# Performance work log

Measured on AMD Instinct MI355X. Metric: run time of the kernel, lower is better.

## Reference

```python
import jax, jax.numpy as jnp
import numpy as np

N_NODES = 100000
N_EDGES = 1600000
NUM_GRAPHS = 4096
HID = 128
F_IN = 11
F_OUT = 19


def setup_inputs() -> dict:
    key = jax.random.key(0)
    ks = jax.random.split(key, 8)
    x = jax.random.normal(ks[0], (N_NODES, F_IN), dtype=jnp.float32)
    edge_src = jax.random.randint(ks[1], (N_EDGES,), 0, N_NODES)
    edge_dst = jax.random.randint(ks[2], (N_EDGES,), 0, N_NODES)
    batch = jnp.sort(jax.random.randint(ks[3], (N_NODES,), 0, NUM_GRAPHS))
    W1 = jax.random.normal(ks[4], (F_IN, HID), dtype=jnp.float32) / np.sqrt(F_IN)
    b1 = jnp.zeros((HID,), dtype=jnp.float32)
    W2 = jax.random.normal(ks[5], (HID, HID), dtype=jnp.float32) / np.sqrt(HID)
    b2 = jnp.zeros((HID,), dtype=jnp.float32)
    Wlin = jax.random.normal(ks[6], (HID, F_OUT), dtype=jnp.float32) / np.sqrt(HID)
    blin = jnp.zeros((F_OUT,), dtype=jnp.float32)
    return {"x": x, "edge_src": edge_src, "edge_dst": edge_dst, "batch": batch,
            "W1": W1, "b1": b1, "W2": W2, "b2": b2, "Wlin": Wlin, "blin": blin}


def _gcn_conv(x, W, b, src, dst, norm, n_nodes):
    # x: [N, Fin] -> h: [N, Fout]; gather-normalize-scatter over edges (self-loops included in src/dst/norm)
    h = x @ W
    msgs = h[src] * norm[:, None]              # [E+N, Fout]
    out = jax.ops.segment_sum(msgs, dst, num_segments=n_nodes)
    return out + b


def reference(x, edge_src, edge_dst, batch, W1, b1, W2, b2, Wlin, blin):
    n = x.shape[0]
    # add self-loops (GCNConv default)
    loops = jnp.arange(n)
    src = jnp.concatenate([edge_src, loops])
    dst = jnp.concatenate([edge_dst, loops])
    # symmetric normalization deg^-1/2[src] * deg^-1/2[dst], deg computed on dst with self-loops
    deg = jax.ops.segment_sum(jnp.ones_like(dst, dtype=x.dtype), dst, num_segments=n)
    dinv = jnp.where(deg > 0, jax.lax.rsqrt(deg), 0.0)
    norm = dinv[src] * dinv[dst]
    h = _gcn_conv(x, W1, b1, src, dst, norm, n)
    h = jax.nn.relu(h)
    h = _gcn_conv(h, W2, b2, src, dst, norm, n)
    # global mean pool over batch assignment
    sums = jax.ops.segment_sum(h, batch, num_segments=NUM_GRAPHS)
    cnts = jax.ops.segment_sum(jnp.ones((n,), dtype=h.dtype), batch, num_segments=NUM_GRAPHS)
    pooled = sums / jnp.maximum(cnts, 1.0)[:, None]   # [NUM_GRAPHS, HID]
    return pooled @ Wlin + blin                       # [NUM_GRAPHS, F_OUT]
```

## Files before the change

kernel.cpp:

```cpp
#include <hip/hip_runtime.h>
#include <hip/hip_fp16.h>

#define N_NODES 100000
#define N_EDGES 1600000
#define NUM_G   4096
#define HID     128
#define F_IN    11
#define F_PAD   16
#define F_OUT   19

#define NB      256
#define KPB     391
#define BCAP    8192
#define GCAP    1024
#define P01_EPB 2048
#define NREG    8
#define REGW    12500
#define GPB     4
#define NAGG    782
#define CH_G    8

__device__ inline void acc_row_f16(float* acc, uint4 u, float w) {
    const __half2* hp = (const __half2*)&u;
#pragma unroll
    for (int i = 0; i < 4; ++i) {
        acc[2 * i]     += __half2float(__low2half(hp[i]))  * w;
        acc[2 * i + 1] += __half2float(__high2half(hp[i])) * w;
    }
}
__device__ inline void add_row_f16(float* acc, uint4 u) {
    const __half2* hp = (const __half2*)&u;
#pragma unroll
    for (int i = 0; i < 4; ++i) {
        acc[2 * i]     += __half2float(__low2half(hp[i]));
        acc[2 * i + 1] += __half2float(__high2half(hp[i]));
    }
}

__global__ void p1_place(const int* __restrict__ src, const int* __restrict__ dst,
                         int* __restrict__ bcur, unsigned int* __restrict__ ebuf) {
    __shared__ int h[NB];
    __shared__ int base[NB];
    h[threadIdx.x] = 0;
    __syncthreads();
    unsigned int pk[8]; int bn[8];
    int b0 = blockIdx.x * P01_EPB;
    int e8 = b0 + threadIdx.x * 8;
    if (e8 + 8 <= N_EDGES) {
        int4 s0 = *(const int4*)(src + e8);
        int4 s1 = *(const int4*)(src + e8 + 4);
        int4 d0 = *(const int4*)(dst + e8);
        int4 d1 = *(const int4*)(dst + e8 + 4);
        int ss[8] = { s0.x, s0.y, s0.z, s0.w, s1.x, s1.y, s1.z, s1.w };
        int dd[8] = { d0.x, d0.y, d0.z, d0.w, d1.x, d1.y, d1.z, d1.w };
#pragma unroll
        for (int k = 0; k < 8; ++k) {
            bn[k] = dd[k] / KPB;
            pk[k] = ((unsigned)ss[k] << 9) | (unsigned)(dd[k] - bn[k] * KPB);
        }
    } else {
#pragma unroll
        for (int k = 0; k < 8; ++k) {
            int e = e8 + k;
            if (e < N_EDGES) {
                int d = dst[e];
                bn[k] = d / KPB;
                pk[k] = ((unsigned)src[e] << 9) | (unsigned)(d - bn[k] * KPB);
            } else bn[k] = -1;
        }
    }
#pragma unroll
    for (int k = 0; k < 8; ++k)
        if (bn[k] >= 0) atomicAdd(&h[bn[k]], 1);
    __syncthreads();
    {
        int c = h[threadIdx.x];
        base[threadIdx.x] = c ? atomicAdd(&bcur[threadIdx.x], c) : 0;
    }
    __syncthreads();
    h[threadIdx.x] = 0;
    __syncthreads();
#pragma unroll
    for (int k = 0; k < 8; ++k) {
        if (bn[k] >= 0) {
            int r = atomicAdd(&h[bn[k]], 1);
            ebuf[(size_t)bn[k] * BCAP + base[bn[k]] + r] = pk[k];
        }
    }
}

__global__ void p2_build(const unsigned int* __restrict__ ebuf, const int* __restrict__ bcur,
                         const float* __restrict__ x,
                         int* __restrict__ row_ptr, int* __restrict__ deg,
                         int* __restrict__ col, float* __restrict__ wd,
                         float* __restrict__ dinv, __half* __restrict__ xp) {
    __shared__ int hist[512];
    __shared__ float ldinv[512];
    __shared__ int wsum[8];
    __shared__ int woff[8];
    int b  = blockIdx.x;
    int t  = threadIdx.x;
    int dbase = b * KPB;
    int nd = N_NODES - dbase; if (nd > KPB) nd = KPB;
    hist[t] = 0;
    __syncthreads();
    int e0 = b * BCAP;
    int e1 = e0 + bcur[b];
    for (int e = e0 + t; e < e1; e += 512)
        atomicAdd(&hist[ebuf[e] & 511u], 1);
    __syncthreads();
    int v = hist[t];
    int lane = t & 63, wv = t >> 6;
    int sv = v;
#pragma unroll
    for (int off = 1; off < 64; off <<= 1) {
        int n = __shfl_up(sv, off, 64);
        if (lane >= off) sv += n;
    }
    if (lane == 63) wsum[wv] = sv;
    __syncthreads();
    if (t == 0) {
        int run = 0;
#pragma unroll
        for (int w = 0; w < 8; ++w) { woff[w] = run; run += wsum[w]; }
    }
    __syncthreads();
    int excl = sv - v + woff[wv];
    float di = rsqrtf(1.0f + (float)v);
    ldinv[t] = di;
    if (t < nd) {
        row_ptr[dbase + t] = e0 + excl;
        deg[dbase + t]     = v;
        dinv[dbase + t]    = di;
    }
    __syncthreads();
    hist[t] = e0 + excl;
    __syncthreads();
    for (int e = e0 + t; e < e1; e += 512) {
        unsigned int w = ebuf[e];
        int dl = (int)(w & 511u);
        int pos = atomicAdd(&hist[dl], 1);
        col[pos] = (int)(w >> 9);
        wd[pos]  = ldinv[dl];
    }
    for (int idx = t; idx < nd * F_PAD; idx += 512) {
        int vl = idx >> 4, f = idx & 15;
        int gv = dbase + vl;
        xp[(size_t)gv * F_PAD + f] =
            __float2half_rn((f < F_IN) ? ldinv[vl] * x[(size_t)gv * F_IN + f] : 0.f);
    }
}

__global__ void agg_es8(const __half* __restrict__ xp, const int* __restrict__ row_ptr,
                        const int* __restrict__ deg, const int* __restrict__ col,
                        const float* __restrict__ dinv,
                        const float* __restrict__ W1, const float* __restrict__ b1,
                        __half* __restrict__ Bh,
                        const int* __restrict__ batch, const float* __restrict__ wd,
                        uint2* __restrict__ ewp, int* __restrict__ gro,
                        int* __restrict__ gb) {
    __shared__ float xs[128][F_PAD];
    __shared__ float W1s[F_IN * HID];
    __shared__ float b1s[HID];
    __shared__ float ds[128];
    __shared__ int cnt[NREG];
    __shared__ int cur[NREG];
    __shared__ int range[2];
    int tid = threadIdx.x;

    if (blockIdx.x < NAGG) {
        for (int i = tid; i < F_IN * HID; i += 256) W1s[i] = W1[i];
        if (tid < HID) b1s[tid] = b1[tid];
        const uint4* xp4 = (const uint4*)xp;
        int v0   = blockIdx.x * 128;
        int v    = v0 + (tid >> 1);
        int lane = tid & 1;
        if (v < N_NODES) {
            if (lane == 0) ds[tid >> 1] = dinv[v];
            float a[8];
#pragma unroll
            for (int k = 0; k < 8; ++k) a[k] = 0.f;
            add_row_f16(a, xp4[(size_t)v * 2 + lane]);
            int j = row_ptr[v], end = j + deg[v];
            for (; j + 3 < end; j += 4) {
                int s0 = col[j], s1 = col[j + 1], s2 = col[j + 2], s3 = col[j + 3];
                uint4 u0 = xp4[(size_t)s0 * 2 + lane];
                uint4 u1 = xp4[(size_t)s1 * 2 + lane];
                uint4 u2 = xp4[(size_t)s2 * 2 + lane];
                uint4 u3 = xp4[(size_t)s3 * 2 + lane];
                add_row_f16(a, u0); add_row_f16(a, u1);
                add_row_f16(a, u2); add_row_f16(a, u3);
            }
            for (; j < end; ++j)
                add_row_f16(a, xp4[(size_t)col[j] * 2 + lane]);
#pragma unroll
            for (int k = 0; k < 8; ++k) xs[tid >> 1][lane * 8 + k] = a[k];
        }
        __syncthreads();
        int jf   = tid & 127;
        int half = tid >> 7;
        int nmax = N_NODES - v0; if (nmax > 128) nmax = 128;
        for (int n = half; n < nmax; n += 2) {
            float a = 0.f;
#pragma unroll
            for (int k = 0; k < F_IN; ++k) a += xs[n][k] * W1s[k * HID + jf];
            float dv = ds[n];
            float h = fmaxf(dv * a + b1s[jf], 0.f);
            Bh[(size_t)(v0 + n) * HID + jf] = __float2half_rn(dv * h);
        }
    } else {
        int g = blockIdx.x - NAGG;
        if (tid < NREG) cnt[tid] = 0;
        if (tid < 2) {
            int tgt = g + tid;
            int lo = 0, hi = N_NODES;
            while (lo < hi) { int m = (lo + hi) >> 1; if (batch[m] < tgt) lo = m + 1; else hi = m; }
            range[tid] = lo;
        }
        __syncthreads();
        int r0 = range[0], r1 = range[1];
        if (tid == 0) {
            gb[g] = r0;
            if (g == NUM_G - 1) gb[NUM_G] = N_NODES;
        }
        int bb0 = 0, bb1 = -1;
        if (r1 > r0) { bb0 = r0 / KPB; bb1 = (r1 - 1) / KPB; }
        for (int bb = bb0; bb <= bb1; ++bb) {
            int vlo = r0 > bb * KPB ? r0 : bb * KPB;
            int vhi = r1 < bb * KPB + KPB ? r1 : bb * KPB + KPB;
            int ee0 = row_ptr[vlo];
            int ee1 = row_ptr[vhi - 1] + deg[vhi - 1];
            for (int e = ee0 + tid; e < ee1; e += 256)
                atomicAdd(&cnt[(unsigned)col[e] / REGW], 1);
        }
        for (int v = r0 + tid; v < r1; v += 256)
            atomicAdd(&cnt[(unsigned)v / REGW], 1);
        __syncthreads();
        if (tid == 0) {
            int run = g * GCAP;
#pragma unroll
            for (int p = 0; p < NREG; ++p) {
                gro[g * 9 + p] = run;
                cur[p] = run;
                run += cnt[p];
            }
            gro[g * 9 + 8] = run;
        }
        __syncthreads();
        for (int bb = bb0; bb <= bb1; ++bb) {
            int vlo = r0 > bb * KPB ? r0 : bb * KPB;
            int vhi = r1 < bb * KPB + KPB ? r1 : bb * KPB + KPB;
            int ee0 = row_ptr[vlo];
            int ee1 = row_ptr[vhi - 1] + deg[vhi - 1];
            for (int e = ee0 + tid; e < ee1; e += 256) {
                int s = col[e];
                int pos = atomicAdd(&cur[(unsigned)s / REGW], 1);
                ewp[pos] = make_uint2((unsigned)s, __float_as_uint(wd[e]));
            }
        }
        for (int v = r0 + tid; v < r1; v += 256) {
            int pos = atomicAdd(&cur[(unsigned)v / REGW], 1);
            ewp[pos] = make_uint2((unsigned)v, __float_as_uint(dinv[v]));
        }
    }
}

__global__ void pool_gather(const __half* __restrict__ Bh,
                            const int* __restrict__ gro,
                            const uint2* __restrict__ ewp,
                            float* __restrict__ part) {
    __shared__ float red[32][HID + 4];
    int b    = blockIdx.x;
    int gset = b >> 3;
    int p    = b & 7;
    int tid  = threadIdx.x;
    int grp  = tid >> 3;
    int lane = tid & 7;
    int g    = gset * GPB + (grp >> 3);
    int q    = grp & 7;
    const uint4* B4 = (const uint4*)Bh;
    float acc[16];
#pragma unroll
    for (int k = 0; k < 16; ++k) acc[k] = 0.f;

    int e0 = gro[g * 9 + p], e1 = gro[g * 9 + p + 1];
    int e = e0 + q;
    for (; e + 24 < e1; e += 32) {
        uint2 q0 = ewp[e], q1 = ewp[e + 8], q2 = ewp[e + 16], q3 = ewp[e + 24];
        uint4 u00 = B4[(size_t)q0.x * 16 + lane];
        uint4 u01 = B4[(size_t)q0.x * 16 + 8 + lane];
        uint4 u10 = B4[(size_t)q1.x * 16 + lane];
        uint4 u11 = B4[(size_t)q1.x * 16 + 8 + lane];
        uint4 u20 = B4[(size_t)q2.x * 16 + lane];
        uint4 u21 = B4[(size_t)q2.x * 16 + 8 + lane];
        uint4 u30 = B4[(size_t)q3.x * 16 + lane];
        uint4 u31 = B4[(size_t)q3.x * 16 + 8 + lane];
        float w0 = __uint_as_float(q0.y), w1 = __uint_as_float(q1.y);
        float w2 = __uint_as_float(q2.y), w3 = __uint_as_float(q3.y);
        acc_row_f16(acc,     u00, w0);
        acc_row_f16(acc + 8, u01, w0);
        acc_row_f16(acc,     u10, w1);
        acc_row_f16(acc + 8, u11, w1);
        acc_row_f16(acc,     u20, w2);
        acc_row_f16(acc + 8, u21, w2);
        acc_row_f16(acc,     u30, w3);
        acc_row_f16(acc + 8, u31, w3);
    }
    for (; e < e1; e += 8) {
        uint2 q0 = ewp[e];
        uint4 u00 = B4[(size_t)q0.x * 16 + lane];
        uint4 u01 = B4[(size_t)q0.x * 16 + 8 + lane];
        float w0 = __uint_as_float(q0.y);
        acc_row_f16(acc,     u00, w0);
        acc_row_f16(acc + 8, u01, w0);
    }
#pragma unroll
    for (int k = 0; k < 8; ++k) red[grp][lane * 8 + k]      = acc[k];
#pragma unroll
    for (int k = 0; k < 8; ++k) red[grp][64 + lane * 8 + k] = acc[8 + k];
    __syncthreads();
    for (int i = tid; i < GPB * HID; i += 256) {
        int gg = i >> 7, f = i & 127;
        int rb = gg * 8;
        float s = 0.f;
#pragma unroll
        for (int r = 0; r < 8; ++r) s += red[rb + r][f];
        part[(size_t)((gset * GPB + gg) * NREG + p) * HID + f] = s;
    }
}

__global__ void combine_head(const float* __restrict__ part, const int* __restrict__ gb,
                             const float* __restrict__ W2, const float* __restrict__ b2,
                             const float* __restrict__ Wlin, const float* __restrict__ blin,
                             float* __restrict__ out) {
    __shared__ float r[CH_G][HID];
    __shared__ float tt[CH_G][HID + 4];
    __shared__ float bsc[CH_G];
    int g0  = blockIdx.x * CH_G;
    int tid = threadIdx.x;
    int f   = tid & 127;
    int gh  = tid >> 7;
    int q0  = gh * 4;
#pragma unroll
    for (int c = 0; c < 4; ++c) {
        int gg = q0 + c;
        int g  = g0 + gg;
        float s = 0.f;
#pragma unroll
        for (int p = 0; p < NREG; ++p) s += part[(size_t)(g * NREG + p) * HID + f];
        int cnt = gb[g + 1] - gb[g];
        float inv = (cnt > 0) ? 1.0f / (float)cnt : 0.f;
        r[gg][f] = s * inv;
        if (f == 0) bsc[gg] = (cnt > 0) ? 1.0f : 0.f;
    }
    __syncthreads();
    float bf = b2[f];
    float t0 = bf * bsc[q0];
    float t1 = bf * bsc[q0 + 1];
    float t2 = bf * bsc[q0 + 2];
    float t3 = bf * bsc[q0 + 3];
#pragma unroll 4
    for (int k = 0; k < HID; ++k) {
        float w = W2[k * HID + f];
        t0 += r[q0][k] * w;
        t1 += r[q0 + 1][k] * w;
        t2 += r[q0 + 2][k] * w;
        t3 += r[q0 + 3][k] * w;
    }
    tt[q0][f]     = t0;
    tt[q0 + 1][f] = t1;
    tt[q0 + 2][f] = t2;
    tt[q0 + 3][f] = t3;
    __syncthreads();
    if (tid < CH_G * F_OUT) {
        int gg = tid / F_OUT;
        int fo = tid - gg * F_OUT;
        float o = blin[fo];
#pragma unroll 8
        for (int k = 0; k < HID; ++k) o += tt[gg][k] * Wlin[k * F_OUT + fo];
        out[(size_t)(g0 + gg) * F_OUT + fo] = o;
    }
}

extern "C" void kernel_launch(void* const* d_in, const int* in_sizes, int n_in,
                              void* d_out, int out_size, void* d_ws, size_t ws_size,
                              hipStream_t stream) {
    const float* x    = (const float*)d_in[0];
    const int*   esrc = (const int*)  d_in[1];
    const int*   edst = (const int*)  d_in[2];
    const int*   batch= (const int*)  d_in[3];
    const float* W1   = (const float*)d_in[4];
    const float* b1   = (const float*)d_in[5];
    const float* W2   = (const float*)d_in[6];
    const float* b2   = (const float*)d_in[7];
    const float* Wlin = (const float*)d_in[8];
    const float* blin = (const float*)d_in[9];
    float* out = (float*)d_out;

    char* p = (char*)d_ws;
    float*        dinv    = (float*)p;        p += sizeof(float) * N_NODES;
    __half*       xp      = (__half*)p;       p += sizeof(__half) * (size_t)N_NODES * F_PAD;
    __half*       Bh      = (__half*)p;       p += sizeof(__half) * (size_t)N_NODES * HID;
    unsigned int* ebuf    = (unsigned int*)p; p += sizeof(unsigned int) * (size_t)NB * BCAP;
    int*          col     = (int*)p;          p += sizeof(int) * (size_t)NB * BCAP;
    float*        wd      = (float*)p;        p += sizeof(float) * (size_t)NB * BCAP;
    int*          deg     = (int*)p;          p += sizeof(int) * N_NODES;
    uint2*        ewp     = (uint2*)p;        p += sizeof(uint2) * (size_t)NUM_G * GCAP;
    float*        part    = (float*)p;        p += sizeof(float) * (size_t)NUM_G * NREG * HID;
    int*          row_ptr = (int*)p;          p += sizeof(int) * (N_NODES + 4);
    int*          gb      = (int*)p;          p += sizeof(int) * (NUM_G + 4);
    int*          gro     = (int*)p;          p += sizeof(int) * (NUM_G * 9 + 4);
    int*          bcur    = (int*)p;          p += sizeof(int) * NB;

    const int nblk_e = (N_EDGES + P01_EPB - 1) / P01_EPB;

    hipMemsetAsync(bcur, 0, sizeof(int) * NB, stream);
    p1_place<<<nblk_e, 256, 0, stream>>>(esrc, edst, bcur, ebuf);
    p2_build<<<NB, 512, 0, stream>>>(ebuf, bcur, x, row_ptr, deg, col, wd, dinv, xp);

    agg_es8<<<NAGG + NUM_G, 256, 0, stream>>>(xp, row_ptr, deg, col, dinv, W1, b1, Bh,
                                              batch, wd, ewp, gro, gb);

    pool_gather<<<(NUM_G / GPB) * NREG, 256, 0, stream>>>(Bh, gro, ewp, part);

    combine_head<<<NUM_G / CH_G, 256, 0, stream>>>(part, gb, W2, b2, Wlin, blin, out);
}
```

Measured before the change: 239.1 us.

## Stage bucketed edges in LDS for coalesced writes; widen build kernel to 1024 threads

The edge placement kernel now sorts its 2048 edges by bucket in shared memory, using a block-wide prefix scan, and then writes them out in contiguous runs per bucket. The old code scattered each edge straight to global memory. The goal is to cut uncoalesced global writes, at the cost of an extra shared-memory pass and more LDS use per block. The CSR build kernel also goes from 512 to 1024 threads, with the 512-bin scan limited to the first 512 threads, to get more parallelism on the edge loops.

```diff
diff --git a/kernel.cpp b/kernel.cpp
--- a/kernel.cpp
+++ b/kernel.cpp
@@ -40,12 +40,18 @@
 __global__ void p1_place(const int* __restrict__ src, const int* __restrict__ dst,
                          int* __restrict__ bcur, unsigned int* __restrict__ ebuf) {
     __shared__ int h[NB];
-    __shared__ int base[NB];
-    h[threadIdx.x] = 0;
+    __shared__ int lbase[NB];
+    __shared__ int gbase[NB];
+    __shared__ int wsum4[4];
+    __shared__ int total_s;
+    __shared__ unsigned int stage[P01_EPB];
+    __shared__ unsigned char sbuck[P01_EPB];
+    int tid = threadIdx.x;
+    h[tid] = 0;
     __syncthreads();
     unsigned int pk[8]; int bn[8];
     int b0 = blockIdx.x * P01_EPB;
-    int e8 = b0 + threadIdx.x * 8;
+    int e8 = b0 + tid * 8;
     if (e8 + 8 <= N_EDGES) {
         int4 s0 = *(const int4*)(src + e8);
         int4 s1 = *(const int4*)(src + e8 + 4);
@@ -73,19 +79,39 @@
     for (int k = 0; k < 8; ++k)
         if (bn[k] >= 0) atomicAdd(&h[bn[k]], 1);
     __syncthreads();
-    {
-        int c = h[threadIdx.x];
-        base[threadIdx.x] = c ? atomicAdd(&bcur[threadIdx.x], c) : 0;
-    }
-    __syncthreads();
-    h[threadIdx.x] = 0;
+    int c = h[tid];
+    gbase[tid] = c ? atomicAdd(&bcur[tid], c) : 0;
+    int lane = tid & 63, wv = tid >> 6;
+    int sv = c;
+#pragma unroll
+    for (int off = 1; off < 64; off <<= 1) {
+        int n = __shfl_up(sv, off, 64);
+        if (lane >= off) sv += n;
+    }
+    if (lane == 63) wsum4[wv] = sv;
+    __syncthreads();
+    int woff = 0;
+    for (int w = 0; w < wv; ++w) woff += wsum4[w];
+    int excl = sv - c + woff;
+    lbase[tid] = excl;
+    if (tid == NB - 1) total_s = excl + c;
+    __syncthreads();
+    h[tid] = 0;
     __syncthreads();
 #pragma unroll
     for (int k = 0; k < 8; ++k) {
         if (bn[k] >= 0) {
             int r = atomicAdd(&h[bn[k]], 1);
-            ebuf[(size_t)bn[k] * BCAP + base[bn[k]] + r] = pk[k];
-        }
+            int p_ = lbase[bn[k]] + r;
+            stage[p_] = pk[k];
+            sbuck[p_] = (unsigned char)bn[k];
+        }
+    }
+    __syncthreads();
+    int total = total_s;
+    for (int i = tid; i < total; i += NB) {
+        int b = sbuck[i];
+        ebuf[(size_t)b * BCAP + gbase[b] + (i - lbase[b])] = stage[i];
     }
 }
 
@@ -102,22 +128,25 @@
     int t  = threadIdx.x;
     int dbase = b * KPB;
     int nd = N_NODES - dbase; if (nd > KPB) nd = KPB;
-    hist[t] = 0;
+    if (t < 512) hist[t] = 0;
     __syncthreads();
     int e0 = b * BCAP;
     int e1 = e0 + bcur[b];
-    for (int e = e0 + t; e < e1; e += 512)
+    for (int e = e0 + t; e < e1; e += 1024)
         atomicAdd(&hist[ebuf[e] & 511u], 1);
     __syncthreads();
-    int v = hist[t];
+    int v = 0, sv = 0;
     int lane = t & 63, wv = t >> 6;
-    int sv = v;
-#pragma unroll
-    for (int off = 1; off < 64; off <<= 1) {
-        int n = __shfl_up(sv, off, 64);
-        if (lane >= off) sv += n;
-    }
-    if (lane == 63) wsum[wv] = sv;
+    if (t < 512) {
+        v = hist[t];
+        sv = v;
+#pragma unroll
+        for (int off = 1; off < 64; off <<= 1) {
+            int n = __shfl_up(sv, off, 64);
+            if (lane >= off) sv += n;
+        }
+        if (lane == 63) wsum[wv] = sv;
+    }
     __syncthreads();
     if (t == 0) {
         int run = 0;
@@ -125,25 +154,28 @@
         for (int w = 0; w < 8; ++w) { woff[w] = run; run += wsum[w]; }
     }
     __syncthreads();
-    int excl = sv - v + woff[wv];
-    float di = rsqrtf(1.0f + (float)v);
-    ldinv[t] = di;
-    if (t < nd) {
-        row_ptr[dbase + t] = e0 + excl;
-        deg[dbase + t]     = v;
-        dinv[dbase + t]    = di;
-    }
-    __syncthreads();
-    hist[t] = e0 + excl;
-    __syncthreads();
-    for (int e = e0 + t; e < e1; e += 512) {
+    int excl = 0;
+    if (t < 512) {
+        excl = sv - v + woff[wv];
+        float di = rsqrtf(1.0f + (float)v);
+        ldinv[t] = di;
+        if (t < nd) {
+            row_ptr[dbase + t] = e0 + excl;
+            deg[dbase + t]     = v;
+            dinv[dbase + t]    = di;
+        }
+    }
+    __syncthreads();
+    if (t < 512) hist[t] = e0 + excl;
+    __syncthreads();
+    for (int e = e0 + t; e < e1; e += 1024) {
         unsigned int w = ebuf[e];
         int dl = (int)(w & 511u);
         int pos = atomicAdd(&hist[dl], 1);
         col[pos] = (int)(w >> 9);
         wd[pos]  = ldinv[dl];
     }
-    for (int idx = t; idx < nd * F_PAD; idx += 512) {
+    for (int idx = t; idx < nd * F_PAD; idx += 1024) {
         int vl = idx >> 4, f = idx & 15;
         int gv = dbase + vl;
         xp[(size_t)gv * F_PAD + f] =
@@ -416,7 +448,7 @@
 
     hipMemsetAsync(bcur, 0, sizeof(int) * NB, stream);
     p1_place<<<nblk_e, 256, 0, stream>>>(esrc, edst, bcur, ebuf);
-    p2_build<<<NB, 512, 0, stream>>>(ebuf, bcur, x, row_ptr, deg, col, wd, dinv, xp);
+    p2_build<<<NB, 1024, 0, stream>>>(ebuf, bcur, x, row_ptr, deg, col, wd, dinv, xp);
 
     agg_es8<<<NAGG + NUM_G, 256, 0, stream>>>(xp, row_ptr, deg, col, dinv, W1, b1, Bh,
                                               batch, wd, ewp, gro, gb);
```

After: 230.0 us. 1.04x faster.
